# Kernel optimization log

Hardware: AMD Instinct MI355X
Metric: run time of the kernel (lower is better)

## Reference

```python
import jax, jax.numpy as jnp
import numpy as np

S, B, D, NH, DH, L, V, DI = 1024, 4, 768, 12, 64, 4, 32000, 3072


def layer_norm(x, g, b, eps=1e-5):
    mu = jnp.mean(x, axis=-1, keepdims=True)
    var = jnp.mean((x - mu) ** 2, axis=-1, keepdims=True)
    return (x - mu) * jax.lax.rsqrt(var + eps) * g + b


def sinusoid_pos_emb():
    # PositionalEmbedding: ger(pos_seq, inv_freq) then [sin, cos]
    pos_seq = jnp.arange(S - 1, -1, -1, dtype=jnp.float32)
    inv_freq = 1.0 / (10000.0 ** (jnp.arange(0.0, D, 2.0) / D))
    si = pos_seq[:, None] * inv_freq[None, :]
    return jnp.concatenate([jnp.sin(si), jnp.cos(si)], axis=-1)  # (S, D)


def setup_inputs() -> dict:
    key = jax.random.key(0)
    ks = jax.random.split(key, 16)
    w = 0.02
    inp = jax.random.randint(ks[0], (S, B), 0, V)
    word_emb = jax.random.normal(ks[1], (V, D)) * w
    Wq = jax.random.normal(ks[2], (L, D, D)) * w
    Wkv = jax.random.normal(ks[3], (L, 2 * D, D)) * w
    Wo = jax.random.normal(ks[4], (L, D, D)) * w
    ln1_g = jnp.ones((L, D)); ln1_b = jnp.zeros((L, D))
    ffW1 = jax.random.normal(ks[5], (L, DI, D)) * w
    ffb1 = jnp.zeros((L, DI))
    ffW2 = jax.random.normal(ks[6], (L, D, DI)) * w
    ffb2 = jnp.zeros((L, D))
    ln2_g = jnp.ones((L, D)); ln2_b = jnp.zeros((L, D))
    # pre-populated InfiniAttn memory state; norm kept strictly positive
    memory = jax.random.normal(ks[7], (L, B, NH, DH, DH)) * jnp.sqrt(jnp.float32(S))
    mem_norm = jax.random.uniform(ks[8], (L, B, NH, DH)) * S + 0.5 * S
    return dict(inp=inp, word_emb=word_emb, Wq=Wq, Wkv=Wkv, Wo=Wo,
                ln1_g=ln1_g, ln1_b=ln1_b, ffW1=ffW1, ffb1=ffb1,
                ffW2=ffW2, ffb2=ffb2, ln2_g=ln2_g, ln2_b=ln2_b,
                memory=memory, mem_norm=mem_norm)


def reference(inp, word_emb, Wq, Wkv, Wo, ln1_g, ln1_b, ffW1, ffb1, ffW2, ffb2,
              ln2_g, ln2_b, memory, mem_norm):
    emb_scale = D ** 0.5
    h = word_emb[inp] * emb_scale + sinusoid_pos_emb()[:, None, :]  # (S,B,D)
    causal = jnp.triu(jnp.ones((S, S), dtype=bool), k=1)  # mask j > i
    scale = 1.0 / DH ** 0.5
    gate = jax.nn.sigmoid(jnp.float32(0.01))  # sigmoid(beta), beta_eps=0.01 (buffer)
    neg_inf = jnp.finfo(h.dtype).min
    new_mems, new_norms = [], []
    for l in range(L):
        q = (h @ Wq[l].T).reshape(S, B, NH, DH)
        kv = h @ Wkv[l].T
        k, v = jnp.split(kv, 2, axis=-1)
        k = k.reshape(S, B, NH, DH)
        v = v.reshape(S, B, NH, DH)
        score = jnp.einsum('ibnd,jbnd->ijbn', q, k) * scale
        score = jnp.where(causal[:, :, None, None], neg_inf, score)
        prob = jax.nn.softmax(score, axis=1)
        attn_vec = jnp.einsum('ijbn,jbnd->ibnd', prob, v).reshape(S, B, NH * DH)
        # NOTE: original calls _update_memory(head_q, head_v, head_k), i.e. K=v, V=k
        Qb = jnp.swapaxes(q, 0, 1)  # (B,S,n,d)
        Kb = jnp.swapaxes(v, 0, 1)
        Vb = jnp.swapaxes(k, 0, 1)
        cQ = jax.nn.elu(Qb) + 1.0
        cK = jax.nn.elu(Kb) + 1.0
        # memory retrieval (detached in the original)
        num = jnp.einsum('bsnk,bnkv->bsnv', cQ, memory[l])
        den = jnp.einsum('bsnk,bnk->bsn', cQ, mem_norm[l])[..., None]
        content_A = jax.lax.stop_gradient(num / den)  # (B,S,n,d)
        # memory update with delta trick (no_grad in the original)
        numK = jnp.einsum('bsnk,bnkv->bsnv', cK, memory[l])
        denK = jnp.einsum('bsnk,bnk->bsn', cK, mem_norm[l])[..., None]
        delta = numK / denK
        new_mems.append(jax.lax.stop_gradient(
            memory[l] + jnp.einsum('bsnk,bsnv->bnkv', cK, Vb - delta)))
        new_norms.append(jax.lax.stop_gradient(mem_norm[l] + cK.sum(axis=1)))
        # gated injection of memory content into local attention output
        attn_vec = gate * jnp.swapaxes(content_A, 0, 1).reshape(S, B, NH * DH) \
                   + (1.0 - gate) * attn_vec
        out = layer_norm(h + attn_vec @ Wo[l].T, ln1_g[l], ln1_b[l])
        core = jax.nn.relu(out @ ffW1[l].T + ffb1[l]) @ ffW2[l].T + ffb2[l]
        h = layer_norm(out + core, ln2_g[l], ln2_b[l])
    return h, jnp.stack(new_mems), jnp.stack(new_norms)
```

## Files before the change

### kernel.cpp

```cpp
#include <hip/hip_runtime.h>
#include <hip/hip_bf16.h>
#include <math.h>

#define S 1024
#define B 4
#define Dm 768
#define NH 12
#define DH 64
#define NL 4
#define DI 3072
#define QS 2304
#define MU_CHUNK 8
#define NROW (S * B * NH)

typedef __hip_bfloat16 bf16;
typedef short bf16x8 __attribute__((ext_vector_type(8)));
typedef float f32x4 __attribute__((ext_vector_type(4)));

__device__ __forceinline__ float b2f(bf16 x) { return __bfloat162float(x); }
__device__ __forceinline__ bf16 f2b(float x) { return __float2bfloat16(x); }

__device__ __forceinline__ float ldv(const float* p, size_t i) { return p[i]; }
__device__ __forceinline__ float ldv(const bf16* p, size_t i) { return b2f(p[i]); }

__device__ __forceinline__ float wave_sum(float x) {
  #pragma unroll
  for (int off = 32; off > 0; off >>= 1) x += __shfl_xor(x, off, 64);
  return x;
}

typedef const __attribute__((address_space(1))) unsigned int guint;
typedef __attribute__((address_space(3))) unsigned int luint;
__device__ __forceinline__ void async_cp16(const void* g, void* l) {
  __builtin_amdgcn_global_load_lds((guint*)g, (luint*)l, 16, 0, 0);
}

__global__ void embed_kernel(const int* __restrict__ inp, const float* __restrict__ wemb,
                             float* __restrict__ h, bf16* __restrict__ hb) {
  int idx = blockIdx.x * blockDim.x + threadIdx.x;
  if (idx >= S * B * Dm) return;
  int d = idx % Dm;
  int sb = idx / Dm;
  int b = sb % B;
  int s = sb / B;
  int tok = inp[s * B + b];
  float e = wemb[(size_t)tok * Dm + d] * 27.712812921102035f;
  float ps = (float)(S - 1 - s);
  float pe;
  if (d < Dm / 2) {
    float invf = expf(-(2.0f * (float)d / (float)Dm) * 9.210340371976184f);
    pe = sinf(ps * invf);
  } else {
    int j = d - Dm / 2;
    float invf = expf(-(2.0f * (float)j / (float)Dm) * 9.210340371976184f);
    pe = cosf(ps * invf);
  }
  float val = e + pe;
  h[idx] = val;
  hb[idx] = f2b(val);
}

#define SEG_QKV 1769472
#define SEG_WO  2359296
#define SEG_W1  4718592
#define SEG_END 7077888
__global__ void convw_kernel(const float* __restrict__ Wq, const float* __restrict__ Wkv,
                             const float* __restrict__ Wo, const float* __restrict__ W1,
                             const float* __restrict__ W2, bf16* __restrict__ dst) {
  int idx = (blockIdx.x * blockDim.x + threadIdx.x) * 4;
  if (idx >= SEG_END) return;
  const float* src;
  if (idx < SEG_QKV) {
    src = (idx < 589824) ? Wq + idx : Wkv + (idx - 589824);
  } else if (idx < SEG_WO) {
    src = Wo + (idx - SEG_QKV);
  } else if (idx < SEG_W1) {
    src = W1 + (idx - SEG_WO);
  } else {
    src = W2 + (idx - SEG_W1);
  }
  float4 f = *(const float4*)src;
  bf16 b0 = f2b(f.x), b1 = f2b(f.y), b2 = f2b(f.z), b3 = f2b(f.w);
  unsigned short o[4];
  o[0] = *(unsigned short*)&b0; o[1] = *(unsigned short*)&b1;
  o[2] = *(unsigned short*)&b2; o[3] = *(unsigned short*)&b3;
  *(uint2*)((unsigned short*)dst + idx) = *(uint2*)o;
}

template <int MREP, int RELU, int SPLITK, typename OT>
__global__ __launch_bounds__(256) void gemm_async(const bf16* __restrict__ A,
                                                  const bf16* __restrict__ W,
                                                  const float* __restrict__ bias,
                                                  OT* __restrict__ C,
                                                  int ldc, int K) {
  constexpr int BM = MREP * 32;
  __shared__ __align__(16) unsigned short Asm[2][BM * 32];
  __shared__ __align__(16) unsigned short Bsm[2][128 * 32];
  const int t = threadIdx.x;
  const int w = t >> 6, lane = t & 63;
  const int col = lane & 15, quad = lane >> 4;
  const int wm = w >> 1, wn = w & 1;

  int bx = blockIdx.x, by = blockIdx.y;
  {
    const int nwg = gridDim.x * gridDim.y;
    if ((nwg & 7) == 0) {
      int orig = by * gridDim.x + bx;
      int cpx = nwg >> 3;
      int wg2 = (orig & 7) * cpx + (orig >> 3);
      bx = wg2 % gridDim.x;
      by = wg2 / gridDim.x;
    }
  }
  const int m0 = by * BM, n0 = bx * 128;
  const int Kc = K / SPLITK;
  const int kbeg = (SPLITK > 1) ? blockIdx.z * Kc : 0;

  const bf16* aSrc = A + (size_t)(m0 + w * 16 + col) * K + kbeg + quad * 8;
  const bf16* bSrc = W + (size_t)(n0 + w * 16 + col) * K + kbeg + quad * 8;

  const f32x4 zf = {0.0f, 0.0f, 0.0f, 0.0f};
  f32x4 acc[MREP][4];
  #pragma unroll
  for (int mt = 0; mt < MREP; mt++)
    #pragma unroll
    for (int nt = 0; nt < 4; nt++) acc[mt][nt] = zf;

  #pragma unroll
  for (int i = 0; i < MREP / 2; i++)
    async_cp16(aSrc + (size_t)i * 64 * K, &Asm[0][i * 2048 + w * 512]);
  #pragma unroll
  for (int i = 0; i < 2; i++)
    async_cp16(bSrc + (size_t)i * 64 * K, &Bsm[0][i * 2048 + w * 512]);
  __syncthreads();

  int cur = 0;
  for (int kk = 32; kk < Kc; kk += 32) {
    #pragma unroll
    for (int i = 0; i < MREP / 2; i++)
      async_cp16(aSrc + kk + (size_t)i * 64 * K, &Asm[cur ^ 1][i * 2048 + w * 512]);
    #pragma unroll
    for (int i = 0; i < 2; i++)
      async_cp16(bSrc + kk + (size_t)i * 64 * K, &Bsm[cur ^ 1][i * 2048 + w * 512]);
    bf16x8 af[MREP], bfr[4];
    #pragma unroll
    for (int mt = 0; mt < MREP; mt++)
      af[mt] = *(const bf16x8*)&Asm[cur][(wm * MREP + mt) * 512 + lane * 8];
    #pragma unroll
    for (int nt = 0; nt < 4; nt++)
      bfr[nt] = *(const bf16x8*)&Bsm[cur][(wn * 4 + nt) * 512 + lane * 8];
    #pragma unroll
    for (int mt = 0; mt < MREP; mt++)
      #pragma unroll
      for (int nt = 0; nt < 4; nt++)
        acc[mt][nt] = __builtin_amdgcn_mfma_f32_16x16x32_bf16(af[mt], bfr[nt],
                                                              acc[mt][nt], 0, 0, 0);
    __syncthreads();
    cur ^= 1;
  }
  {
    bf16x8 af[MREP], bfr[4];
    #pragma unroll
    for (int mt = 0; mt < MREP; mt++)
      af[mt] = *(const bf16x8*)&Asm[cur][(wm * MREP + mt) * 512 + lane * 8];
    #pragma unroll
    for (int nt = 0; nt < 4; nt++)
      bfr[nt] = *(const bf16x8*)&Bsm[cur][(wn * 4 + nt) * 512 + lane * 8];
    #pragma unroll
    for (int mt = 0; mt < MREP; mt++)
      #pragma unroll
      for (int nt = 0; nt < 4; nt++)
        acc[mt][nt] = __builtin_amdgcn_mfma_f32_16x16x32_bf16(af[mt], bfr[nt],
                                                              acc[mt][nt], 0, 0, 0);
  }

  OT* Cb = C;
  if (SPLITK > 1)
    Cb = C + (size_t)blockIdx.z * gridDim.y * BM * ldc;
  #pragma unroll
  for (int nt = 0; nt < 4; nt++) {
    const int colg = n0 + wn * 64 + nt * 16 + col;
    const float bv = bias ? bias[colg] : 0.0f;
    #pragma unroll
    for (int mt = 0; mt < MREP; mt++) {
      #pragma unroll
      for (int r = 0; r < 4; r++) {
        const int row = m0 + wm * (MREP * 16) + mt * 16 + quad * 4 + r;
        float val = acc[mt][nt][r] + bv;
        if (RELU) val = fmaxf(val, 0.0f);
        if constexpr (__is_same(OT, float)) {
          Cb[(size_t)row * ldc + colg] = val;
        } else {
          Cb[(size_t)row * ldc + colg] = f2b(val);
        }
      }
    }
  }
}

__global__ __launch_bounds__(256) void vtrans_kernel(const bf16* __restrict__ v,
                                                     bf16* __restrict__ vt) {
  const int s0 = blockIdx.x * 64;
  const int bn = blockIdx.y;
  const int b = bn / NH, n = bn % NH;
  const int t = threadIdx.x;
  __shared__ __align__(16) unsigned short Tl[64 * 72];
  const unsigned short* vp = (const unsigned short*)v;
  {
    int jj = t >> 2, d0 = (t & 3) * 16;
    size_t gb = ((size_t)(s0 + jj) * B + b) * QS + n * DH + d0;
    unsigned short tv[16];
    *(uint4*)tv = *(const uint4*)(vp + gb);
    *(uint4*)(tv + 8) = *(const uint4*)(vp + gb + 8);
    #pragma unroll
    for (int x = 0; x < 16; x++) Tl[(d0 + x) * 72 + jj] = tv[x];
  }
  __syncthreads();
  {
    int d = t >> 2, so = (t & 3) * 16;
    unsigned short* op = (unsigned short*)vt + ((size_t)bn * 64 + d) * S + s0 + so;
    *(uint4*)op = *(const uint4*)&Tl[d * 72 + so];
    *(uint4*)(op + 8) = *(const uint4*)&Tl[d * 72 + so + 8];
  }
}

template <int SPLIT, int VT>
__global__ __launch_bounds__(256) void attn_flash(const bf16* __restrict__ q,
                                                  const bf16* __restrict__ k,
                                                  const bf16* __restrict__ v,
                                                  const bf16* __restrict__ vtg,
                                                  bf16* __restrict__ att,
                                                  bf16* __restrict__ po0,
                                                  bf16* __restrict__ po1,
                                                  float* __restrict__ pml) {
  const int it = blockIdx.x;
  const int bn = blockIdx.y;
  const int b = bn / NH, n = bn % NH;
  const int t = threadIdx.x;
  const int w = t >> 6, lane = t & 63;
  const int col = lane & 15, quad = lane >> 4;
  const int i0 = it * 64;

  int jbeg = 0, jend = it + 1;
  if (SPLIT == 2) {
    const int half = (it + 2) >> 1;
    if (blockIdx.z == 0) jend = half; else jbeg = half;
    if (jbeg >= jend) return;
  }

  __shared__ __align__(16) unsigned short Kt[64 * 72];
  __shared__ __align__(16) unsigned short Vt[64 * 72];
  __shared__ __align__(16) unsigned short Pw[64 * 72];

  const unsigned short* qp = (const unsigned short*)q;
  const unsigned short* kp = (const unsigned short*)k;
  const unsigned short* vp = (const unsigned short*)v;
  const unsigned short* vtp = (const unsigned short*)vtg;

  bf16x8 aq[2];
  {
    size_t qb = ((size_t)(i0 + w * 16 + col) * B + b) * QS + n * DH + quad * 8;
    aq[0] = *(const bf16x8*)(qp + qb);
    aq[1] = *(const bf16x8*)(qp + qb + 32);
  }

  const f32x4 zf = {0.0f, 0.0f, 0.0f, 0.0f};
  float mrow[4], lrow[4];
  f32x4 o[4];
  #pragma unroll
  for (int r = 0; r < 4; r++) { mrow[r] = -1e30f; lrow[r] = 0.0f; }
  #pragma unroll
  for (int db = 0; db < 4; db++) o[db] = zf;

  const int jj = t >> 2;
  const int d0 = (t & 3) << 4;

  uint4 rk0, rk1, rv0, rv1;
  {
    size_t gb = ((size_t)(jbeg * 64 + jj) * B + b) * QS + n * DH + d0;
    rk0 = *(const uint4*)(kp + gb); rk1 = *(const uint4*)(kp + gb + 8);
    if constexpr (VT) {
      size_t gv = ((size_t)bn * 64 + jj) * S + jbeg * 64 + d0;
      rv0 = *(const uint4*)(vtp + gv); rv1 = *(const uint4*)(vtp + gv + 8);
    } else {
      rv0 = *(const uint4*)(vp + gb); rv1 = *(const uint4*)(vp + gb + 8);
    }
  }

  for (int jt = jbeg; jt < jend; jt++) {
    const int j0 = jt * 64;
    __syncthreads();
    {
      *(uint4*)&Kt[jj * 72 + d0] = rk0;
      *(uint4*)&Kt[jj * 72 + d0 + 8] = rk1;
      if constexpr (VT) {
        *(uint4*)&Vt[jj * 72 + d0] = rv0;
        *(uint4*)&Vt[jj * 72 + d0 + 8] = rv1;
      } else {
        unsigned short tv[16];
        *(uint4*)tv = rv0;
        *(uint4*)(tv + 8) = rv1;
        #pragma unroll
        for (int x = 0; x < 16; x++) Vt[(d0 + x) * 72 + jj] = tv[x];
      }
    }
    __syncthreads();
    if (jt + 1 < jend) {
      size_t gb = ((size_t)((jt + 1) * 64 + jj) * B + b) * QS + n * DH + d0;
      rk0 = *(const uint4*)(kp + gb); rk1 = *(const uint4*)(kp + gb + 8);
      if constexpr (VT) {
        size_t gv = ((size_t)bn * 64 + jj) * S + (jt + 1) * 64 + d0;
        rv0 = *(const uint4*)(vtp + gv); rv1 = *(const uint4*)(vtp + gv + 8);
      } else {
        rv0 = *(const uint4*)(vp + gb); rv1 = *(const uint4*)(vp + gb + 8);
      }
    }

    f32x4 sf[4];
    #pragma unroll
    for (int nb = 0; nb < 4; nb++) sf[nb] = zf;
    #pragma unroll
    for (int ks = 0; ks < 2; ks++) {
      #pragma unroll
      for (int nb = 0; nb < 4; nb++) {
        bf16x8 kb = *(const bf16x8*)&Kt[(nb * 16 + col) * 72 + ks * 32 + quad * 8];
        sf[nb] = __builtin_amdgcn_mfma_f32_16x16x32_bf16(aq[ks], kb, sf[nb], 0, 0, 0);
      }
    }

    const bool diag = (jt == it);
    #pragma unroll
    for (int r = 0; r < 4; r++) {
      const int irow = i0 + w * 16 + quad * 4 + r;
      float sv[4];
      #pragma unroll
      for (int nb = 0; nb < 4; nb++) {
        float s = sf[nb][r] * 0.125f;
        if (diag && (j0 + nb * 16 + col) > irow) s = -1e30f;
        sv[nb] = s;
      }
      float rm = fmaxf(fmaxf(sv[0], sv[1]), fmaxf(sv[2], sv[3]));
      #pragma unroll
      for (int off = 8; off > 0; off >>= 1) rm = fmaxf(rm, __shfl_xor(rm, off, 64));
      const float mn = fmaxf(mrow[r], rm);
      const float alpha = __expf(mrow[r] - mn);
      mrow[r] = mn;
      float ps = 0.0f;
      #pragma unroll
      for (int nb = 0; nb < 4; nb++) {
        float p = __expf(sv[nb] - mn);
        ps += p;
        bf16 hb = f2b(p);
        Pw[(w * 16 + quad * 4 + r) * 72 + nb * 16 + col] = *(unsigned short*)&hb;
      }
      #pragma unroll
      for (int off = 8; off > 0; off >>= 1) ps += __shfl_xor(ps, off, 64);
      lrow[r] = lrow[r] * alpha + ps;
      #pragma unroll
      for (int db = 0; db < 4; db++) o[db][r] *= alpha;
    }

    #pragma unroll
    for (int ks = 0; ks < 2; ks++) {
      bf16x8 pa = *(const bf16x8*)&Pw[(w * 16 + col) * 72 + ks * 32 + quad * 8];
      #pragma unroll
      for (int db = 0; db < 4; db++) {
        bf16x8 vb = *(const bf16x8*)&Vt[(db * 16 + col) * 72 + ks * 32 + quad * 8];
        o[db] = __builtin_amdgcn_mfma_f32_16x16x32_bf16(pa, vb, o[db], 0, 0, 0);
      }
    }
  }

  if (SPLIT == 1) {
    unsigned short* ap = (unsigned short*)att;
    #pragma unroll
    for (int r = 0; r < 4; r++) {
      const int irow = i0 + w * 16 + quad * 4 + r;
      const float inv = 1.0f / lrow[r];
      size_t ob = ((size_t)irow * B + b) * Dm + n * DH + col;
      #pragma unroll
      for (int db = 0; db < 4; db++) {
        bf16 hb = f2b(o[db][r] * inv);
        ap[ob + db * 16] = *(unsigned short*)&hb;
      }
    }
  } else {
    unsigned short* pp = (unsigned short*)(blockIdx.z ? po1 : po0);
    float* pm = pml + (size_t)blockIdx.z * 2 * NROW;
    float* pl = pm + NROW;
    #pragma unroll
    for (int r = 0; r < 4; r++) {
      const int irow = i0 + w * 16 + quad * 4 + r;
      const float inv = 1.0f / lrow[r];
      size_t ob = ((size_t)irow * B + b) * Dm + n * DH + col;
      #pragma unroll
      for (int db = 0; db < 4; db++) {
        bf16 hb = f2b(o[db][r] * inv);
        pp[ob + db * 16] = *(unsigned short*)&hb;
      }
      if (col == 0) {
        int rix = (irow * B + b) * NH + n;
        pm[rix] = mrow[r];
        pl[rix] = lrow[r];
      }
    }
  }
}

__global__ void attn_comb(const bf16* __restrict__ po0, const bf16* __restrict__ po1,
                          const float* __restrict__ pml, bf16* __restrict__ att) {
  size_t i4 = ((size_t)blockIdx.x * blockDim.x + threadIdx.x) * 4;
  if (i4 >= (size_t)S * B * Dm) return;
  int sb = (int)(i4 / Dm);
  int dd = (int)(i4 % Dm);
  int srow = sb / B;
  int it = srow >> 6;
  uint2 a0 = *(const uint2*)((const unsigned short*)po0 + i4);
  if (it == 0) {
    *(uint2*)((unsigned short*)att + i4) = a0;
    return;
  }
  uint2 a1 = *(const uint2*)((const unsigned short*)po1 + i4);
  int rix = sb * NH + (dd >> 6);
  float m0 = pml[rix],            l0 = pml[NROW + rix];
  float m1 = pml[2 * NROW + rix], l1 = pml[3 * NROW + rix];
  float M = fmaxf(m0, m1);
  float w0 = l0 * __expf(m0 - M), w1 = l1 * __expf(m1 - M);
  float inv = 1.0f / (w0 + w1);
  const unsigned short* p0 = (const unsigned short*)&a0;
  const unsigned short* p1 = (const unsigned short*)&a1;
  unsigned short o[4];
  #pragma unroll
  for (int j = 0; j < 4; j++) {
    float val = (w0 * b2f(*(const bf16*)&p0[j]) + w1 * b2f(*(const bf16*)&p1[j])) * inv;
    bf16 hb = f2b(val);
    o[j] = *(unsigned short*)&hb;
  }
  *(uint2*)((unsigned short*)att + i4) = *(uint2*)o;
}

__global__ __launch_bounds__(256) void meminfer_mfma(const bf16* __restrict__ qkv,
                                                     const float* __restrict__ mem,
                                                     const float* __restrict__ mnorm,
                                                     bf16* __restrict__ att,
                                                     bf16* __restrict__ vd) {
  const int s0 = blockIdx.x * 64;
  const int bn = blockIdx.y;
  const int b = bn / NH, n = bn % NH;
  const int t = threadIdx.x;
  const int w = t >> 6, lane = t & 63;
  const int col = lane & 15, quad = lane >> 4;

  __shared__ __align__(16) unsigned short CQ[4096];
  __shared__ __align__(16) unsigned short CK[4096];
  __shared__ __align__(16) unsigned short Bm[5120];

  const unsigned short* qp = (const unsigned short*)qkv;

  {
    int r = t >> 2;
    int k0 = (t & 3) * 16;
    size_t gb = ((size_t)(s0 + r) * B + b) * QS + n * DH + k0;
    int abase = (r >> 4) * 1024 + (k0 >> 5) * 512 + ((k0 & 31) >> 3) * 128 + (r & 15) * 8;
    unsigned short tq[16], tv[16], oq[16], ov[16];
    *(uint4*)tq = *(const uint4*)(qp + gb);
    *(uint4*)(tq + 8) = *(const uint4*)(qp + gb + 8);
    *(uint4*)tv = *(const uint4*)(qp + gb + 1536);
    *(uint4*)(tv + 8) = *(const uint4*)(qp + gb + 1536 + 8);
    #pragma unroll
    for (int i = 0; i < 16; i++) {
      float fq = b2f(*(const bf16*)&tq[i]);
      float fv = b2f(*(const bf16*)&tv[i]);
      float eq = fq > 0.0f ? fq + 1.0f : __expf(fq);
      float ev = fv > 0.0f ? fv + 1.0f : __expf(fv);
      bf16 bq = f2b(eq), bv2 = f2b(ev);
      oq[i] = *(unsigned short*)&bq;
      ov[i] = *(unsigned short*)&bv2;
    }
    *(bf16x8*)&CQ[abase] = *(bf16x8*)oq;
    *(bf16x8*)&CQ[abase + 128] = *(bf16x8*)(oq + 8);
    *(bf16x8*)&CK[abase] = *(bf16x8*)ov;
    *(bf16x8*)&CK[abase + 128] = *(bf16x8*)(ov + 8);
  }
  {
    int v = t & 63, kb = (t >> 6) * 16;
    const float* mp = mem + (size_t)bn * DH * DH;
    #pragma unroll
    for (int i = 0; i < 16; i++) {
      int k = kb + i;
      bf16 mb = f2b(mp[(size_t)k * DH + v]);
      int addr = (v >> 4) * 1024 + (k >> 5) * 512 + ((k & 31) >> 3) * 128 + (v & 15) * 8 + (k & 7);
      Bm[addr] = *(unsigned short*)&mb;
    }
  }
  {
    int a = t * 4;
    int m = (a >> 3) & 15;
    int kk = (a >> 9) * 32 + ((a >> 7) & 3) * 8 + (a & 7);
    unsigned short vals[4] = {0, 0, 0, 0};
    if (m == 0) {
      const float* np = mnorm + (size_t)bn * DH;
      #pragma unroll
      for (int j = 0; j < 4; j++) {
        bf16 nb = f2b(np[kk + j]);
        vals[j] = *(unsigned short*)&nb;
      }
    }
    *(uint2*)&Bm[4096 + a] = *(uint2*)vals;
  }
  __syncthreads();

  const f32x4 zf = {0.0f, 0.0f, 0.0f, 0.0f};
  f32x4 aq[5], ak[5];
  #pragma unroll
  for (int nb = 0; nb < 5; nb++) { aq[nb] = zf; ak[nb] = zf; }
  #pragma unroll
  for (int ks = 0; ks < 2; ks++) {
    bf16x8 fq = *(const bf16x8*)&CQ[w * 1024 + ks * 512 + lane * 8];
    bf16x8 fk = *(const bf16x8*)&CK[w * 1024 + ks * 512 + lane * 8];
    #pragma unroll
    for (int nb = 0; nb < 5; nb++) {
      bf16x8 bm = *(const bf16x8*)&Bm[nb * 1024 + ks * 512 + lane * 8];
      aq[nb] = __builtin_amdgcn_mfma_f32_16x16x32_bf16(fq, bm, aq[nb], 0, 0, 0);
      ak[nb] = __builtin_amdgcn_mfma_f32_16x16x32_bf16(fk, bm, ak[nb], 0, 0, 0);
    }
  }

  const float gate = 1.0f / (1.0f + expf(-0.01f));
  unsigned short* ap = (unsigned short*)att;
  unsigned short* vp2 = (unsigned short*)vd;
  #pragma unroll
  for (int r = 0; r < 4; r++) {
    const int srow = s0 + w * 16 + quad * 4 + r;
    const float denq = __shfl(aq[4][r], lane & 48, 64);
    const float denk = __shfl(ak[4][r], lane & 48, 64);
    const size_t bd = ((size_t)srow * B + b) * Dm + n * DH + col;
    const size_t bq = ((size_t)srow * B + b) * QS + 768 + n * DH + col;
    #pragma unroll
    for (int nb = 0; nb < 4; nb++) {
      float content = aq[nb][r] / denq;
      float delta = ak[nb][r] / denk;
      float attv = b2f(*(const bf16*)&ap[bd + nb * 16]);
      bf16 ao = f2b(gate * content + (1.0f - gate) * attv);
      ap[bd + nb * 16] = *(unsigned short*)&ao;
      float kvv = b2f(*(const bf16*)&qp[bq + nb * 16]);
      bf16 vo = f2b(kvv - delta);
      vp2[bd + nb * 16] = *(unsigned short*)&vo;
    }
  }
}

__global__ void memupd_kernel(const bf16* __restrict__ qkv, const bf16* __restrict__ vd,
                              float* __restrict__ part, float* __restrict__ pnorm) {
  int bn = blockIdx.x % (B * NH);
  int c = blockIdx.x / (B * NH);
  int b = bn / NH, n = bn % NH;
  int t = threadIdx.x;
  int k = t >> 2;
  int v0 = (t & 3) * 16;
  __shared__ float ckl[8][DH];
  __shared__ float vdl[8][DH];
  float acc[16];
  #pragma unroll
  for (int j = 0; j < 16; j++) acc[j] = 0.0f;
  float nsum = 0.0f;
  const int sBeg = c * (S / MU_CHUNK), sEnd = sBeg + S / MU_CHUNK;
  for (int s0 = sBeg; s0 < sEnd; s0 += 8) {
    #pragma unroll
    for (int i2 = 0; i2 < 2; i2++) {
      int idx = t + i2 * 256;
      int sp = idx >> 6, dd = idx & 63;
      int gq = ((s0 + sp) * B + b) * QS + 1536 + n * DH + dd;
      int gd = ((s0 + sp) * B + b) * Dm + n * DH + dd;
      float vv = b2f(qkv[gq]);
      ckl[sp][dd] = vv > 0.0f ? vv + 1.0f : expf(vv);
      vdl[sp][dd] = b2f(vd[gd]);
    }
    __syncthreads();
    #pragma unroll
    for (int sp = 0; sp < 8; sp++) {
      float cc = ckl[sp][k];
      if ((t & 3) == 0) nsum += cc;
      #pragma unroll
      for (int j = 0; j < 16; j++) acc[j] += cc * vdl[sp][v0 + j];
    }
    __syncthreads();
  }
  float* prow = part + (size_t)c * (B * NH * DH * DH) + (size_t)bn * DH * DH;
  #pragma unroll
  for (int j4 = 0; j4 < 4; j4++) {
    float4 o;
    o.x = acc[j4 * 4 + 0]; o.y = acc[j4 * 4 + 1];
    o.z = acc[j4 * 4 + 2]; o.w = acc[j4 * 4 + 3];
    *(float4*)&prow[k * DH + v0 + j4 * 4] = o;
  }
  if ((t & 3) == 0) pnorm[(size_t)c * (B * NH * DH) + bn * DH + k] = nsum;
}

__global__ void memred_kernel(const float* __restrict__ mem, const float* __restrict__ mnorm,
                              const float* __restrict__ part, const float* __restrict__ pnorm,
                              float* __restrict__ out_mem, float* __restrict__ out_norm) {
  const int MEMN = B * NH * DH * DH;
  int i = blockIdx.x * blockDim.x + threadIdx.x;
  if (i < MEMN / 4) {
    int i4 = i * 4;
    float4 a = *(const float4*)(mem + i4);
    #pragma unroll
    for (int c = 0; c < MU_CHUNK; c++) {
      float4 p = *(const float4*)(part + (size_t)c * MEMN + i4);
      a.x += p.x; a.y += p.y; a.z += p.z; a.w += p.w;
    }
    *(float4*)(out_mem + i4) = a;
  } else {
    int j4 = (i - MEMN / 4) * 4;
    if (j4 < B * NH * DH) {
      float4 a = *(const float4*)(mnorm + j4);
      #pragma unroll
      for (int c = 0; c < MU_CHUNK; c++) {
        float4 p = *(const float4*)(pnorm + (size_t)c * (B * NH * DH) + j4);
        a.x += p.x; a.y += p.y; a.z += p.z; a.w += p.w;
      }
      *(float4*)(out_norm + j4) = a;
    }
  }
}

template <typename TX, typename TY>
__global__ void addln_kernel(const TX* __restrict__ x, const TY* __restrict__ y,
                             const float* __restrict__ g, const float* __restrict__ bb,
                             float* __restrict__ outf, bf16* __restrict__ outb) {
  int row = blockIdx.x;
  int t = threadIdx.x;
  float vals[3];
  float sum = 0.0f, sq = 0.0f;
  #pragma unroll
  for (int i = 0; i < 3; i++) {
    size_t idx = (size_t)row * Dm + t + i * 256;
    float vv = ldv(x, idx) + ldv(y, idx);
    vals[i] = vv;
    sum += vv;
    sq += vv * vv;
  }
  sum = wave_sum(sum);
  sq = wave_sum(sq);
  __shared__ float s1[4], s2[4];
  int w = t >> 6, lane = t & 63;
  if (lane == 0) { s1[w] = sum; s2[w] = sq; }
  __syncthreads();
  if (t == 0) {
    s1[0] = s1[0] + s1[1] + s1[2] + s1[3];
    s2[0] = s2[0] + s2[1] + s2[2] + s2[3];
  }
  __syncthreads();
  sum = s1[0]; sq = s2[0];
  float mu = sum / 768.0f;
  float var = sq / 768.0f - mu * mu;
  float rs = rsqrtf(var + 1e-5f);
  #pragma unroll
  for (int i = 0; i < 3; i++) {
    int d = t + i * 256;
    float o = (vals[i] - mu) * rs * g[d] + bb[d];
    size_t idx = (size_t)row * Dm + d;
    if (outf) outf[idx] = o;
    if (outb) outb[idx] = f2b(o);
  }
}

template <int NSLICE, typename TX>
__global__ void addln_red_kernel(const TX* __restrict__ x, const float* __restrict__ part,
                                 const float* __restrict__ bias,
                                 const float* __restrict__ g, const float* __restrict__ bb,
                                 float* __restrict__ outf, bf16* __restrict__ outb) {
  const size_t SBDc = (size_t)S * B * Dm;
  int row = blockIdx.x;
  int t = threadIdx.x;
  float vals[3];
  float sum = 0.0f, sq = 0.0f;
  #pragma unroll
  for (int i = 0; i < 3; i++) {
    int d = t + i * 256;
    size_t idx = (size_t)row * Dm + d;
    float y = part[idx];
    #pragma unroll
    for (int z = 1; z < NSLICE; z++) y += part[(size_t)z * SBDc + idx];
    if (bias) y += bias[d];
    float vv = ldv(x, idx) + y;
    vals[i] = vv;
    sum += vv;
    sq += vv * vv;
  }
  sum = wave_sum(sum);
  sq = wave_sum(sq);
  __shared__ float s1[4], s2[4];
  int w = t >> 6, lane = t & 63;
  if (lane == 0) { s1[w] = sum; s2[w] = sq; }
  __syncthreads();
  if (t == 0) {
    s1[0] = s1[0] + s1[1] + s1[2] + s1[3];
    s2[0] = s2[0] + s2[1] + s2[2] + s2[3];
  }
  __syncthreads();
  sum = s1[0]; sq = s2[0];
  float mu = sum / 768.0f;
  float var = sq / 768.0f - mu * mu;
  float rs = rsqrtf(var + 1e-5f);
  #pragma unroll
  for (int i = 0; i < 3; i++) {
    int d = t + i * 256;
    float o = (vals[i] - mu) * rs * g[d] + bb[d];
    size_t idx = (size_t)row * Dm + d;
    if (outf) outf[idx] = o;
    if (outb) outb[idx] = f2b(o);
  }
}

extern "C" void kernel_launch(void* const* d_in, const int* in_sizes, int n_in,
                              void* d_out, int out_size, void* d_ws, size_t ws_size,
                              hipStream_t stream) {
  (void)in_sizes; (void)n_in; (void)out_size;
  const int*   inp   = (const int*)d_in[0];
  const float* wemb  = (const float*)d_in[1];
  const float* Wq    = (const float*)d_in[2];
  const float* Wkv   = (const float*)d_in[3];
  const float* Wo    = (const float*)d_in[4];
  const float* ln1g  = (const float*)d_in[5];
  const float* ln1b  = (const float*)d_in[6];
  const float* fW1   = (const float*)d_in[7];
  const float* fb1   = (const float*)d_in[8];
  const float* fW2   = (const float*)d_in[9];
  const float* fb2   = (const float*)d_in[10];
  const float* ln2g  = (const float*)d_in[11];
  const float* ln2b  = (const float*)d_in[12];
  const float* mem   = (const float*)d_in[13];
  const float* mnorm = (const float*)d_in[14];

  const size_t SBD = (size_t)S * B * Dm;

  bf16* ws   = (bf16*)d_ws;
  bf16* qkv  = ws;
  bf16* vd   = ws + 3 * SBD;
  bf16* att  = ws + 4 * SBD;
  bf16* hbf  = att;
  bf16* out1 = ws + 5 * SBD;
  bf16* wb   = ws + 6 * SBD;
  bf16* ffm  = ws;
  bf16* tmp  = ws;
  bf16* ff2o = att;
  float* part  = (float*)out1;
  float* pnorm = (float*)(wb + SEG_END);
  float* partg = pnorm + (size_t)MU_CHUNK * B * NH * DH;
  const size_t need = ((size_t)(6 * SBD + SEG_END)) * 2 +
                      ((size_t)MU_CHUNK * B * NH * DH + 3 * SBD) * 4;
  const bool use_splitk = (ws_size >= need);
  bf16* po0 = vd;
  bf16* po1 = out1;
  float* pml = partg;
  bf16* vt  = (bf16*)(partg + 4 * NROW);

  float* h    = (float*)d_out;
  float* outm = h + SBD;
  float* outn = outm + (size_t)NL * B * NH * DH * DH;

  dim3 b256(256);
  embed_kernel<<<dim3((S * B * Dm + 255) / 256), b256, 0, stream>>>(inp, wemb, h, hbf);

  for (int l = 0; l < NL; l++) {
    convw_kernel<<<dim3(SEG_END / 4 / 256), b256, 0, stream>>>(
        Wq + (size_t)l * Dm * Dm, Wkv + (size_t)l * 2 * Dm * Dm,
        Wo + (size_t)l * Dm * Dm, fW1 + (size_t)l * DI * Dm,
        fW2 + (size_t)l * Dm * DI, wb);
    const bf16* wqkv = wb;
    const bf16* wo_b = wb + SEG_QKV;
    const bf16* w1_b = wb + SEG_WO;
    const bf16* w2_b = wb + SEG_W1;
    const float* mem_l = mem + (size_t)l * B * NH * DH * DH;
    const float* mn_l  = mnorm + (size_t)l * B * NH * DH;
    float* outm_l = outm + (size_t)l * B * NH * DH * DH;
    float* outn_l = outn + (size_t)l * B * NH * DH;

    gemm_async<4, 0, 1, bf16><<<dim3(QS / 128, 32), b256, 0, stream>>>(
        hbf, wqkv, nullptr, qkv, QS, Dm);

    if (use_splitk) {
      vtrans_kernel<<<dim3(S / 64, B * NH), b256, 0, stream>>>(qkv + 1536, vt);
      attn_flash<2, 1><<<dim3(S / 64, B * NH, 2), b256, 0, stream>>>(
          qkv, qkv + 768, qkv + 1536, vt, att, po0, po1, pml);
      attn_comb<<<dim3((unsigned)(SBD / 4 / 256)), b256, 0, stream>>>(po0, po1, pml, att);
    } else {
      attn_flash<1, 0><<<dim3(S / 64, B * NH), b256, 0, stream>>>(
          qkv, qkv + 768, qkv + 1536, nullptr, att, nullptr, nullptr, nullptr);
    }
    meminfer_mfma<<<dim3(S / 64, B * NH), b256, 0, stream>>>(qkv, mem_l, mn_l, att, vd);
    memupd_kernel<<<dim3(B * NH * MU_CHUNK), b256, 0, stream>>>(qkv, vd, part, pnorm);
    memred_kernel<<<dim3(771), b256, 0, stream>>>(mem_l, mn_l, part, pnorm, outm_l, outn_l);

    if (use_splitk) {
      gemm_async<4, 0, 3, float><<<dim3(Dm / 128, 32, 3), b256, 0, stream>>>(
          att, wo_b, nullptr, partg, Dm, Dm);
      addln_red_kernel<3, float><<<dim3(S * B), b256, 0, stream>>>(
          h, partg, nullptr, ln1g + l * Dm, ln1b + l * Dm, nullptr, out1);
    } else {
      gemm_async<2, 0, 1, bf16><<<dim3(Dm / 128, 64), b256, 0, stream>>>(
          att, wo_b, nullptr, tmp, Dm, Dm);
      addln_kernel<float, bf16><<<dim3(S * B), b256, 0, stream>>>(
          h, tmp, ln1g + l * Dm, ln1b + l * Dm, nullptr, out1);
    }

    gemm_async<4, 1, 1, bf16><<<dim3(DI / 128, 32), b256, 0, stream>>>(
        out1, w1_b, fb1 + (size_t)l * DI, ffm, DI, Dm);
    if (use_splitk) {
      gemm_async<4, 0, 3, float><<<dim3(Dm / 128, 32, 3), b256, 0, stream>>>(
          ffm, w2_b, nullptr, partg, Dm, DI);
      addln_red_kernel<3, bf16><<<dim3(S * B), b256, 0, stream>>>(
          out1, partg, fb2 + (size_t)l * Dm, ln2g + l * Dm, ln2b + l * Dm, h, hbf);
    } else {
      gemm_async<2, 0, 1, bf16><<<dim3(Dm / 128, 64), b256, 0, stream>>>(
          ffm, w2_b, fb2 + (size_t)l * Dm, ff2o, Dm, DI);
      addln_kernel<bf16, bf16><<<dim3(S * B), b256, 0, stream>>>(
          out1, ff2o, ln2g + l * Dm, ln2b + l * Dm, h, hbf);
    }
  }
}
```

Measured before the change: 1.273 ms.

## Fuse split-KV attention combine into memory retrieval kernel and relax GEMM barriers

The separate attn_comb kernel is removed. Its log-sum-exp merge of the two split-KV attention partials now runs inside meminfer_mfma, which reads po0/po1/pml directly. This saves one full pass over the attention output and one kernel launch per layer. The partial buffers are moved to new workspace regions so they do not alias vd and out1, which the fused kernel writes or needs. Separately, the GEMM main loop replaces __syncthreads with explicit vmcnt waits and s_barrier plus sched_barrier, so the next tile's async loads can stay in flight while MFMAs run. The hand-written wait counts must match the async copy ordering to stay correct.

```diff
diff --git a/kernel.cpp b/kernel.cpp
--- a/kernel.cpp
+++ b/kernel.cpp
@@ -94,6 +94,7 @@
                                                   OT* __restrict__ C,
                                                   int ldc, int K) {
   constexpr int BM = MREP * 32;
+  constexpr int NLD = MREP / 2 + 2;
   __shared__ __align__(16) unsigned short Asm[2][BM * 32];
   __shared__ __align__(16) unsigned short Bsm[2][128 * 32];
   const int t = threadIdx.x;
@@ -132,7 +133,9 @@
   #pragma unroll
   for (int i = 0; i < 2; i++)
     async_cp16(bSrc + (size_t)i * 64 * K, &Bsm[0][i * 2048 + w * 512]);
-  __syncthreads();
+  asm volatile("s_waitcnt vmcnt(0)" ::: "memory");
+  __builtin_amdgcn_s_barrier();
+  __builtin_amdgcn_sched_barrier(0);
 
   int cur = 0;
   for (int kk = 32; kk < Kc; kk += 32) {
@@ -142,6 +145,9 @@
     #pragma unroll
     for (int i = 0; i < 2; i++)
       async_cp16(bSrc + kk + (size_t)i * 64 * K, &Bsm[cur ^ 1][i * 2048 + w * 512]);
+    asm volatile("s_waitcnt vmcnt(%0)" :: "n"(NLD) : "memory");
+    __builtin_amdgcn_s_barrier();
+    __builtin_amdgcn_sched_barrier(0);
     bf16x8 af[MREP], bfr[4];
     #pragma unroll
     for (int mt = 0; mt < MREP; mt++)
@@ -155,10 +161,15 @@
       for (int nt = 0; nt < 4; nt++)
         acc[mt][nt] = __builtin_amdgcn_mfma_f32_16x16x32_bf16(af[mt], bfr[nt],
                                                               acc[mt][nt], 0, 0, 0);
-    __syncthreads();
+    __builtin_amdgcn_sched_barrier(0);
+    __builtin_amdgcn_s_barrier();
+    __builtin_amdgcn_sched_barrier(0);
     cur ^= 1;
   }
   {
+    asm volatile("s_waitcnt vmcnt(0)" ::: "memory");
+    __builtin_amdgcn_s_barrier();
+    __builtin_amdgcn_sched_barrier(0);
     bf16x8 af[MREP], bfr[4];
     #pragma unroll
     for (int mt = 0; mt < MREP; mt++)
@@ -407,43 +418,15 @@
   }
 }
 
-__global__ void attn_comb(const bf16* __restrict__ po0, const bf16* __restrict__ po1,
-                          const float* __restrict__ pml, bf16* __restrict__ att) {
-  size_t i4 = ((size_t)blockIdx.x * blockDim.x + threadIdx.x) * 4;
-  if (i4 >= (size_t)S * B * Dm) return;
-  int sb = (int)(i4 / Dm);
-  int dd = (int)(i4 % Dm);
-  int srow = sb / B;
-  int it = srow >> 6;
-  uint2 a0 = *(const uint2*)((const unsigned short*)po0 + i4);
-  if (it == 0) {
-    *(uint2*)((unsigned short*)att + i4) = a0;
-    return;
-  }
-  uint2 a1 = *(const uint2*)((const unsigned short*)po1 + i4);
-  int rix = sb * NH + (dd >> 6);
-  float m0 = pml[rix],            l0 = pml[NROW + rix];
-  float m1 = pml[2 * NROW + rix], l1 = pml[3 * NROW + rix];
-  float M = fmaxf(m0, m1);
-  float w0 = l0 * __expf(m0 - M), w1 = l1 * __expf(m1 - M);
-  float inv = 1.0f / (w0 + w1);
-  const unsigned short* p0 = (const unsigned short*)&a0;
-  const unsigned short* p1 = (const unsigned short*)&a1;
-  unsigned short o[4];
-  #pragma unroll
-  for (int j = 0; j < 4; j++) {
-    float val = (w0 * b2f(*(const bf16*)&p0[j]) + w1 * b2f(*(const bf16*)&p1[j])) * inv;
-    bf16 hb = f2b(val);
-    o[j] = *(unsigned short*)&hb;
-  }
-  *(uint2*)((unsigned short*)att + i4) = *(uint2*)o;
-}
-
+template <int MERGE>
 __global__ __launch_bounds__(256) void meminfer_mfma(const bf16* __restrict__ qkv,
                                                      const float* __restrict__ mem,
                                                      const float* __restrict__ mnorm,
                                                      bf16* __restrict__ att,
-                                                     bf16* __restrict__ vd) {
+                                                     bf16* __restrict__ vd,
+                                                     const bf16* __restrict__ po0,
+                                                     const bf16* __restrict__ po1,
+                                                     const float* __restrict__ pml) {
   const int s0 = blockIdx.x * 64;
   const int bn = blockIdx.y;
   const int b = bn / NH, n = bn % NH;
@@ -529,6 +512,8 @@
   const float gate = 1.0f / (1.0f + expf(-0.01f));
   unsigned short* ap = (unsigned short*)att;
   unsigned short* vp2 = (unsigned short*)vd;
+  const unsigned short* p0 = (const unsigned short*)po0;
+  const unsigned short* p1 = (const unsigned short*)po1;
   #pragma unroll
   for (int r = 0; r < 4; r++) {
     const int srow = s0 + w * 16 + quad * 4 + r;
@@ -536,11 +521,31 @@
     const float denk = __shfl(ak[4][r], lane & 48, 64);
     const size_t bd = ((size_t)srow * B + b) * Dm + n * DH + col;
     const size_t bq = ((size_t)srow * B + b) * QS + 768 + n * DH + col;
+    float w0 = 1.0f, w1 = 0.0f, invw = 1.0f;
+    if (MERGE && blockIdx.x > 0) {
+      int rix = (srow * B + b) * NH + n;
+      float m0 = pml[rix],            l0 = pml[NROW + rix];
+      float m1 = pml[2 * NROW + rix], l1 = pml[3 * NROW + rix];
+      float M = fmaxf(m0, m1);
+      w0 = l0 * __expf(m0 - M); w1 = l1 * __expf(m1 - M);
+      invw = 1.0f / (w0 + w1);
+    }
     #pragma unroll
     for (int nb = 0; nb < 4; nb++) {
       float content = aq[nb][r] / denq;
       float delta = ak[nb][r] / denk;
-      float attv = b2f(*(const bf16*)&ap[bd + nb * 16]);
+      float attv;
+      if (MERGE) {
+        float a0 = b2f(*(const bf16*)&p0[bd + nb * 16]);
+        if (blockIdx.x > 0) {
+          float a1 = b2f(*(const bf16*)&p1[bd + nb * 16]);
+          attv = (w0 * a0 + w1 * a1) * invw;
+        } else {
+          attv = a0;
+        }
+      } else {
+        attv = b2f(*(const bf16*)&ap[bd + nb * 16]);
+      }
       bf16 ao = f2b(gate * content + (1.0f - gate) * attv);
       ap[bd + nb * 16] = *(unsigned short*)&ao;
       float kvv = b2f(*(const bf16*)&qp[bq + nb * 16]);
@@ -752,10 +757,10 @@
   const size_t need = ((size_t)(6 * SBD + SEG_END)) * 2 +
                       ((size_t)MU_CHUNK * B * NH * DH + 3 * SBD) * 4;
   const bool use_splitk = (ws_size >= need);
-  bf16* po0 = vd;
-  bf16* po1 = out1;
   float* pml = partg;
   bf16* vt  = (bf16*)(partg + 4 * NROW);
+  bf16* po0 = vt + SBD;
+  bf16* po1 = po0 + SBD;
 
   float* h    = (float*)d_out;
   float* outm = h + SBD;
@@ -785,12 +790,14 @@
       vtrans_kernel<<<dim3(S / 64, B * NH), b256, 0, stream>>>(qkv + 1536, vt);
       attn_flash<2, 1><<<dim3(S / 64, B * NH, 2), b256, 0, stream>>>(
           qkv, qkv + 768, qkv + 1536, vt, att, po0, po1, pml);
-      attn_comb<<<dim3((unsigned)(SBD / 4 / 256)), b256, 0, stream>>>(po0, po1, pml, att);
+      meminfer_mfma<1><<<dim3(S / 64, B * NH), b256, 0, stream>>>(
+          qkv, mem_l, mn_l, att, vd, po0, po1, pml);
     } else {
       attn_flash<1, 0><<<dim3(S / 64, B * NH), b256, 0, stream>>>(
           qkv, qkv + 768, qkv + 1536, nullptr, att, nullptr, nullptr, nullptr);
-    }
-    meminfer_mfma<<<dim3(S / 64, B * NH), b256, 0, stream>>>(qkv, mem_l, mn_l, att, vd);
+      meminfer_mfma<0><<<dim3(S / 64, B * NH), b256, 0, stream>>>(
+          qkv, mem_l, mn_l, att, vd, nullptr, nullptr, nullptr);
+    }
     memupd_kernel<<<dim3(B * NH * MU_CHUNK), b256, 0, stream>>>(qkv, vd, part, pnorm);
     memred_kernel<<<dim3(771), b256, 0, stream>>>(mem_l, mn_l, part, pnorm, outm_l, outn_l);
 
```

Measured after the change: 1.280 ms. Within noise of the previous version (+0.5%).
